# Optimization experiments

Measured on AMD Instinct MI355X. Metric: run time of the kernel, lower is better.

## Reference

```python
import jax, jax.numpy as jnp
import numpy as np

VEC, HID, B, S = 1280, 128, 4, 256
EPS = 1e-5


def _ln(x):
    m = x.mean(-1, keepdims=True)
    v = ((x - m) ** 2).mean(-1, keepdims=True)
    return (x - m) / jnp.sqrt(v + EPS)


def _add_attn(q_in, kv_in, Wq, Wk, wv):
    # Additive (Bahdanau) attention: scores[b,i,j] = wv . tanh(q[b,i] + k[b,j])
    q = q_in @ Wq            # [B, Sq, H]
    k = kv_in @ Wk           # [B, Sk, H]
    feat = jnp.tanh(q[:, :, None, :] + k[:, None, :, :])   # [B, Sq, Sk, H]
    scores = jnp.einsum('bijh,h->bij', feat, wv)
    attn = jax.nn.softmax(scores, axis=-1)
    return jnp.einsum('bij,bjd->bid', attn, kv_in)          # values = kv_in


def _res_fc(x, W1, b1, W2, b2):
    return jnp.maximum(x @ W1 + b1, 0.0) @ W2 + b2 + x


def setup_inputs() -> dict:
    key = jax.random.key(0)
    ks = iter(jax.random.split(key, 64))
    d = {
        'X': jax.random.normal(next(ks), (B, S, VEC), dtype=jnp.float32),
        'lys_pos': 100,
    }
    sc = 0.02
    for i in (1, 2, 3, 4):
        d[f'Wq{i}'] = jax.random.normal(next(ks), (VEC, HID), dtype=jnp.float32) * sc
        d[f'Wk{i}'] = jax.random.normal(next(ks), (VEC, HID), dtype=jnp.float32) * sc
        d[f'wv{i}'] = jax.random.normal(next(ks), (HID,), dtype=jnp.float32) * sc
    for i in (1, 2, 3):
        d[f'rW1_{i}'] = jax.random.normal(next(ks), (VEC, HID), dtype=jnp.float32) * sc
        d[f'rb1_{i}'] = jnp.zeros((HID,), dtype=jnp.float32)
        d[f'rW2_{i}'] = jax.random.normal(next(ks), (HID, VEC), dtype=jnp.float32) * sc
        d[f'rb2_{i}'] = jnp.zeros((VEC,), dtype=jnp.float32)
    d['hW1'] = jax.random.normal(next(ks), (VEC, 32), dtype=jnp.float32) * sc
    d['hb1'] = jnp.zeros((32,), dtype=jnp.float32)
    d['hW2'] = jax.random.normal(next(ks), (32, 12), dtype=jnp.float32) * sc
    d['hb2'] = jnp.zeros((12,), dtype=jnp.float32)
    d['hW3'] = jax.random.normal(next(ks), (12, 2), dtype=jnp.float32) * sc
    d['hb3'] = jnp.zeros((2,), dtype=jnp.float32)
    return d


def reference(X, lys_pos,
              Wq1, Wk1, wv1, Wq2, Wk2, wv2, Wq3, Wk3, wv3, Wq4, Wk4, wv4,
              rW1_1, rb1_1, rW2_1, rb2_1,
              rW1_2, rb1_2, rW2_2, rb2_2,
              rW1_3, rb1_3, rW2_3, rb2_3,
              hW1, hb1, hW2, hb2, hW3, hb3):
    X = X.astype(jnp.float32)
    X = _ln(_add_attn(X, X, Wq1, Wk1, wv1) + X)
    X = _res_fc(X, rW1_1, rb1_1, rW2_1, rb2_1)
    X = _ln(_add_attn(X, X, Wq2, Wk2, wv2) + X)
    X = _res_fc(X, rW1_2, rb1_2, rW2_2, rb2_2)
    X = _ln(_add_attn(X, X, Wq3, Wk3, wv3) + X)
    X = _res_fc(X, rW1_3, rb1_3, rW2_3, rb2_3)
    X_lys = X[:, lys_pos, :][:, None, :]                    # [B, 1, VEC]
    X_lys = _ln(_add_attn(X_lys, X, Wq4, Wk4, wv4) + X_lys)
    h = jnp.maximum(X_lys @ hW1 + hb1, 0.0)                 # dropout = identity (eval)
    h = jnp.maximum(h @ hW2 + hb2, 0.0)
    logits = (h @ hW3 + hb3)[:, 0, :]                       # squeeze(1) -> [B, 2]
    return logits
```

## Files before the change

kernel.cpp:

```cpp
#include <hip/hip_runtime.h>


#define DEV __device__ __forceinline__

static constexpr int VEC = 1280;
static constexpr int HID = 128;
static constexpr int BB  = 4;
static constexpr int SS  = 256;
static constexpr int MROWS = BB * SS;
static constexpr int NPART = 8;
static constexpr float INV_VEC = 1.0f / 1280.0f;

DEV float ftanh(float x) {
  float e = __expf(2.0f * x);
  return 1.0f - __fdividef(2.0f, e + 1.0f);
}

DEV float waveSum(float v) {
#pragma unroll
  for (int off = 32; off > 0; off >>= 1) v += __shfl_xor(v, off, 64);
  return v;
}
DEV float waveMax(float v) {
#pragma unroll
  for (int off = 32; off > 0; off >>= 1) v = fmaxf(v, __shfl_xor(v, off, 64));
  return v;
}
DEV float blockSum(float v, float* red) {
  v = waveSum(v);
  int tid = threadIdx.x;
  if ((tid & 63) == 0) red[tid >> 6] = v;
  __syncthreads();
  float r = (red[0] + red[1]) + (red[2] + red[3]);
  __syncthreads();
  return r;
}
DEV float blockMax(float v, float* red) {
  v = waveMax(v);
  int tid = threadIdx.x;
  if ((tid & 63) == 0) red[tid >> 6] = v;
  __syncthreads();
  float r = fmaxf(fmaxf(red[0], red[1]), fmaxf(red[2], red[3]));
  __syncthreads();
  return r;
}

template <int MODE, bool AFUSE, bool ALN, bool OBIAS, bool RESLN, bool RESP,
          bool STATS>
__global__ __launch_bounds__(256) void gemm_k(
    const float* __restrict__ A, long sAb, long aPart,
    const float* __restrict__ B0, const float* __restrict__ B1, int nSplitB,
    long sBb, int ldB,
    float* __restrict__ C, long sCb,
    const float* __restrict__ aBias, const float* __restrict__ oBias,
    const float* __restrict__ res,
    float* __restrict__ Ssum, float* __restrict__ Ssq,
    int N, int K, int kChunk) {
  const int n0 = blockIdx.x * 64;
  const int m0 = blockIdx.y * 64;
  const int z  = blockIdx.z;

  const float* Ab = A + (MODE == 2 ? (long)z * sAb : 0L);
  float*       Cb = C + (MODE >= 1 ? (long)z * sCb : 0L);
  const float* resb = (RESP || RESLN)
                          ? (res + (MODE == 2 ? (long)z * sCb : 0L))
                          : nullptr;
  const float* Bsel;
  int nb;
  if (n0 < nSplitB) { Bsel = B0; nb = n0; } else { Bsel = B1; nb = n0 - nSplitB; }
  if (MODE == 2) Bsel += (long)z * sBb;

  const int kBeg = (MODE == 1) ? z * kChunk : 0;
  const int kEnd = (MODE == 1) ? kBeg + kChunk : K;

  __shared__ float As[16][68];
  __shared__ float Bs[16][68];

  const int tid = threadIdx.x;
  const int tx = tid & 15, ty = tid >> 4;
  const int ar = tid >> 2, ac = (tid & 3) << 2;
  const int br = tid >> 4, bc = (tid & 15) << 2;

  float aMean = 0.0f, aRstd = 1.0f;
  if (ALN) {
    const int rm = m0 + ar;
    const float s = Ssum[rm], q = Ssq[rm];
    aMean = s * INV_VEC;
    aRstd = rsqrtf(q * INV_VEC - aMean * aMean + 1e-5f);
  }

  auto loadA = [&](int kt) -> float4 {
    const size_t off = (size_t)(m0 + ar) * K + kt + ac;
    float4 s = *(const float4*)(Ab + off);
    if (AFUSE) {
#pragma unroll
      for (int p2 = 1; p2 < NPART; ++p2) {
        const float4 t2 = *(const float4*)(Ab + (long)p2 * aPart + off);
        s.x += t2.x; s.y += t2.y; s.z += t2.z; s.w += t2.w;
      }
      const float4 bz = *(const float4*)(aBias + kt + ac);
      s.x = fmaxf(s.x + bz.x, 0.0f);
      s.y = fmaxf(s.y + bz.y, 0.0f);
      s.z = fmaxf(s.z + bz.z, 0.0f);
      s.w = fmaxf(s.w + bz.w, 0.0f);
    }
    if (ALN) {
      s.x = (s.x - aMean) * aRstd;
      s.y = (s.y - aMean) * aRstd;
      s.z = (s.z - aMean) * aRstd;
      s.w = (s.w - aMean) * aRstd;
    }
    return s;
  };
  auto loadB = [&](int kt) -> float4 {
    return *(const float4*)(Bsel + (size_t)(kt + br) * ldB + nb + bc);
  };

  float acc[4][4] = {};
  float4 a4 = loadA(kBeg);
  float4 b4 = loadB(kBeg);

  for (int kt = kBeg; kt < kEnd; kt += 16) {
    __syncthreads();
    As[ac + 0][ar] = a4.x;
    As[ac + 1][ar] = a4.y;
    As[ac + 2][ar] = a4.z;
    As[ac + 3][ar] = a4.w;
    *(float4*)&Bs[br][bc] = b4;
    __syncthreads();
    if (kt + 16 < kEnd) {
      a4 = loadA(kt + 16);
      b4 = loadB(kt + 16);
    }
#pragma unroll
    for (int kk = 0; kk < 16; ++kk) {
      const float4 av = *(const float4*)&As[kk][ty << 2];
      const float4 bv = *(const float4*)&Bs[kk][tx << 2];
      const float a[4] = {av.x, av.y, av.z, av.w};
      const float b[4] = {bv.x, bv.y, bv.z, bv.w};
#pragma unroll
      for (int i = 0; i < 4; ++i)
#pragma unroll
        for (int j = 0; j < 4; ++j) acc[i][j] = fmaf(a[i], b[j], acc[i][j]);
    }
  }

  float rs[4], rq[4];
#pragma unroll
  for (int i = 0; i < 4; ++i) {
    const int m = m0 + (ty << 2) + i;
    float mean = 0.0f, rstd = 1.0f;
    if (RESLN) {
      const float s = Ssum[m], q = Ssq[m];
      mean = s * INV_VEC;
      rstd = rsqrtf(q * INV_VEC - mean * mean + 1e-5f);
    }
    if (STATS) { rs[i] = 0.0f; rq[i] = 0.0f; }
#pragma unroll
    for (int j = 0; j < 4; ++j) {
      const int n = n0 + (tx << 2) + j;
      float v = acc[i][j];
      if (OBIAS) v += oBias[n];
      if (RESP) v += resb[(size_t)m * N + n];
      if (RESLN) v += (resb[(size_t)m * N + n] - mean) * rstd;
      Cb[(size_t)m * N + n] = v;
      if (STATS) { rs[i] += v; rq[i] = fmaf(v, v, rq[i]); }
    }
  }
  if (STATS) {
#pragma unroll
    for (int i = 0; i < 4; ++i) {
      float s = rs[i], q = rq[i];
#pragma unroll
      for (int msk = 1; msk < 16; msk <<= 1) {
        s += __shfl_xor(s, msk, 64);
        q += __shfl_xor(q, msk, 64);
      }
      if ((tid & 15) == 0) {
        const int rowg = (MODE == 2 ? z * SS : 0) + m0 + (ty << 2) + i;
        atomicAdd(&Ssum[rowg], s);
        atomicAdd(&Ssq[rowg], q);
      }
    }
  }
}

__global__ __launch_bounds__(256) void qksum_k(const float* __restrict__ QKp,
                                               long ps,
                                               float* __restrict__ Qd,
                                               float* __restrict__ KT,
                                               float* __restrict__ stats) {
  const int r = blockIdx.x, tid = threadIdx.x;
  if (r < 8) stats[r * 256 + tid] = 0.0f;
  const int b = r >> 8, j = r & 255;
  const size_t off = (size_t)r * 256 + tid;
  float v = 0.0f;
#pragma unroll
  for (int p = 0; p < NPART; ++p) v += QKp[(long)p * ps + off];
  if (tid < 128) {
    Qd[(size_t)r * 128 + tid] = v;
  } else {
    KT[(size_t)b * 32768 + (size_t)(tid - 128) * 256 + j] = v;
  }
}

__global__ __launch_bounds__(256) void scores2_k(const float* __restrict__ Qd,
                                                 const float* __restrict__ KT,
                                                 const float* __restrict__ wv,
                                                 float* __restrict__ attn) {
  const int b = blockIdx.y, i0 = blockIdx.x * 2, tid = threadIdx.x;
  __shared__ float qs[2][128], wvs[128], red[4];
  {
    const int rr = tid >> 7, h = tid & 127;
    qs[rr][h] = Qd[(size_t)(b * 256 + i0 + rr) * 128 + h];
  }
  if (tid < 128) wvs[tid] = wv[tid];
  __syncthreads();

  const float* KTb = KT + (size_t)b * 32768 + tid;
  float s0 = 0.0f, s1 = 0.0f;
#pragma unroll 4
  for (int h = 0; h < 128; h += 4) {
    const float k0 = KTb[(h + 0) * 256];
    const float k1 = KTb[(h + 1) * 256];
    const float k2 = KTb[(h + 2) * 256];
    const float k3 = KTb[(h + 3) * 256];
    const float w0 = wvs[h], w1 = wvs[h + 1], w2 = wvs[h + 2], w3 = wvs[h + 3];
    s0 += w0 * ftanh(qs[0][h] + k0) + w1 * ftanh(qs[0][h + 1] + k1) +
          w2 * ftanh(qs[0][h + 2] + k2) + w3 * ftanh(qs[0][h + 3] + k3);
    s1 += w0 * ftanh(qs[1][h] + k0) + w1 * ftanh(qs[1][h + 1] + k1) +
          w2 * ftanh(qs[1][h + 2] + k2) + w3 * ftanh(qs[1][h + 3] + k3);
  }
  {
    const float mx = blockMax(s0, red);
    const float e = __expf(s0 - mx);
    const float tot = blockSum(e, red);
    attn[(size_t)(b * 256 + i0) * 256 + tid] = e / tot;
  }
  {
    const float mx = blockMax(s1, red);
    const float e = __expf(s1 - mx);
    const float tot = blockSum(e, red);
    attn[(size_t)(b * 256 + i0 + 1) * 256 + tid] = e / tot;
  }
}

__global__ __launch_bounds__(256) void kt4q4_k(const float* __restrict__ K4p,
                                               const float* __restrict__ X3,
                                               const float* __restrict__ Wq4,
                                               const int* __restrict__ lys,
                                               float* __restrict__ KT,
                                               float* __restrict__ q4d) {
  __shared__ float partial[256];
  const int vb = blockIdx.x, tid = threadIdx.x;
  if (vb < 512) {
    const int r = vb * 2 + (tid >> 7), h = tid & 127;
    const int b = r >> 8, j = r & 255;
    const size_t off = (size_t)r * 128 + h;
    float v = 0.0f;
#pragma unroll
    for (int p = 0; p < NPART; ++p) v += K4p[(long)p * 131072 + off];
    KT[(size_t)b * 32768 + (size_t)h * 256 + j] = v;
  } else {
    const int b = vb - 512;
    const int lp = lys[0];
    const float* xr = X3 + (size_t)(b * 256 + lp) * VEC;
    const int h = tid & 127, half = tid >> 7;
    float acc = 0.0f;
    const int k0 = half * 640;
    for (int k = k0; k < k0 + 640; ++k)
      acc = fmaf(xr[k], Wq4[(size_t)k * HID + h], acc);
    partial[tid] = acc;
    __syncthreads();
    if (tid < 128) q4d[b * 128 + tid] = partial[tid] + partial[tid + 128];
  }
}

__global__ __launch_bounds__(256) void pv4s_k(const float* __restrict__ q4d,
                                              const float* __restrict__ KT,
                                              const float* __restrict__ wv4,
                                              const int* __restrict__ lys,
                                              const float* __restrict__ X3,
                                              float* __restrict__ A4) {
  const int b = blockIdx.x & 3, cs = blockIdx.x >> 2, tid = threadIdx.x;
  __shared__ float qs[128], wvs[128], aw[256], red[4];
  const int lp = lys[0];
  if (tid < 128) {
    qs[tid] = q4d[b * 128 + tid];
    wvs[tid] = wv4[tid];
  }
  __syncthreads();
  const float* KTb = KT + (size_t)b * 32768 + tid;
  float s = 0.0f;
#pragma unroll 4
  for (int h = 0; h < 128; h += 4) {
    s += wvs[h + 0] * ftanh(qs[h + 0] + KTb[(h + 0) * 256]);
    s += wvs[h + 1] * ftanh(qs[h + 1] + KTb[(h + 1) * 256]);
    s += wvs[h + 2] * ftanh(qs[h + 2] + KTb[(h + 2) * 256]);
    s += wvs[h + 3] * ftanh(qs[h + 3] + KTb[(h + 3) * 256]);
  }
  const float mx = blockMax(s, red);
  const float e = __expf(s - mx);
  const float tot = blockSum(e, red);
  aw[tid] = e / tot;
  __syncthreads();

  const int c = cs * 256 + tid;
  const float* Xb = X3 + (size_t)b * SS * VEC;
  float acc = 0.0f;
#pragma unroll 8
  for (int j = 0; j < 256; ++j) acc = fmaf(aw[j], Xb[(size_t)j * VEC + c], acc);
  acc += Xb[(size_t)lp * VEC + c];
  A4[b * VEC + c] = acc;
}

__global__ __launch_bounds__(256) void lnhead_k(
    const float* __restrict__ A4,
    const float* __restrict__ hW1, const float* __restrict__ hb1,
    const float* __restrict__ hW2, const float* __restrict__ hb2,
    const float* __restrict__ hW3, const float* __restrict__ hb3,
    float* __restrict__ out) {
  const int b = blockIdx.x, tid = threadIdx.x;
  __shared__ float xrow[1280], partial[256], red[4];
  __shared__ float h1s[32], h2s[12];
  float v[5];
  float sum = 0.0f;
#pragma unroll
  for (int k = 0; k < 5; ++k) {
    v[k] = A4[b * VEC + tid + k * 256];
    sum += v[k];
  }
  sum = blockSum(sum, red);
  const float m = sum * INV_VEC;
  float sq = 0.0f;
#pragma unroll
  for (int k = 0; k < 5; ++k) {
    const float dl = v[k] - m;
    sq += dl * dl;
  }
  sq = blockSum(sq, red);
  const float rstd = rsqrtf(sq * INV_VEC + 1e-5f);
#pragma unroll
  for (int k = 0; k < 5; ++k) xrow[tid + k * 256] = (v[k] - m) * rstd;
  __syncthreads();
  {
    const int n = tid & 31, sl = tid >> 5;
    float p = 0.0f;
    for (int k = sl * 160; k < sl * 160 + 160; ++k)
      p = fmaf(xrow[k], hW1[(size_t)k * 32 + n], p);
    partial[tid] = p;
  }
  __syncthreads();
  if (tid < 32) {
    float t = 0.0f;
#pragma unroll
    for (int s2 = 0; s2 < 8; ++s2) t += partial[s2 * 32 + tid];
    h1s[tid] = fmaxf(t + hb1[tid], 0.0f);
  }
  __syncthreads();
  if (tid < 12) {
    float t = 0.0f;
#pragma unroll
    for (int k = 0; k < 32; ++k) t = fmaf(h1s[k], hW2[k * 12 + tid], t);
    h2s[tid] = fmaxf(t + hb2[tid], 0.0f);
  }
  __syncthreads();
  if (tid < 2) {
    float t = 0.0f;
#pragma unroll
    for (int k = 0; k < 12; ++k) t = fmaf(h2s[k], hW3[k * 2 + tid], t);
    out[b * 2 + tid] = t + hb3[tid];
  }
}

extern "C" void kernel_launch(void* const* d_in, const int* in_sizes, int n_in,
                              void* d_out, int out_size, void* d_ws, size_t ws_size,
                              hipStream_t stream) {
  const float* X = (const float*)d_in[0];
  const int* lys = (const int*)d_in[1];
  const float* Wq[4] = {(const float*)d_in[2], (const float*)d_in[5],
                        (const float*)d_in[8], (const float*)d_in[11]};
  const float* Wk[4] = {(const float*)d_in[3], (const float*)d_in[6],
                        (const float*)d_in[9], (const float*)d_in[12]};
  const float* wv[4] = {(const float*)d_in[4], (const float*)d_in[7],
                        (const float*)d_in[10], (const float*)d_in[13]};
  const float* rW1[3] = {(const float*)d_in[14], (const float*)d_in[18],
                         (const float*)d_in[22]};
  const float* rb1[3] = {(const float*)d_in[15], (const float*)d_in[19],
                         (const float*)d_in[23]};
  const float* rW2[3] = {(const float*)d_in[16], (const float*)d_in[20],
                         (const float*)d_in[24]};
  const float* rb2[3] = {(const float*)d_in[17], (const float*)d_in[21],
                         (const float*)d_in[25]};
  const float* hW1 = (const float*)d_in[26];
  const float* hb1 = (const float*)d_in[27];
  const float* hW2 = (const float*)d_in[28];
  const float* hb2 = (const float*)d_in[29];
  const float* hW3 = (const float*)d_in[30];
  const float* hb3 = (const float*)d_in[31];
  float* out = (float*)d_out;

  float* ws = (float*)d_ws;
  const long QK_PS = 262144;
  const long H_PS  = 131072;
  float* QKp   = ws;
  float* Qd    = QKp + (long)NPART * QK_PS;
  float* KT    = Qd + 131072;
  float* attn  = KT + 131072;
  float* Yraw  = attn + 262144;
  float* Hp    = Yraw + 1310720;
  float* buf0  = Hp + (long)NPART * H_PS;
  float* buf1  = buf0 + 1310720;
  float* stats = buf1 + 1310720;
  float* q4d   = stats + 2048;
  float* A4    = q4d + 512;
  float* Ssum = stats, *Ssq = stats + 1024;

  const int NSPLIT_NONE = 1 << 30;
  const float* P[3] = {X, buf0, buf1};
  float* Q[3] = {buf0, buf1, buf0};

  for (int l = 0; l < 3; ++l) {
    const float* Xin = P[l];
    gemm_k<1, false, false, false, false, false, false>
        <<<dim3(4, 16, NPART), 256, 0, stream>>>(
            Xin, 0, 0, Wq[l], Wk[l], HID, 0, HID, QKp, QK_PS, nullptr, nullptr,
            nullptr, nullptr, nullptr, 256, VEC, 160);
    qksum_k<<<dim3(MROWS), 256, 0, stream>>>(QKp, QK_PS, Qd, KT, stats);
    scores2_k<<<dim3(128, BB), 256, 0, stream>>>(Qd, KT, wv[l], attn);
    gemm_k<2, false, false, false, false, true, true>
        <<<dim3(20, 4, BB), 256, 0, stream>>>(
            attn, (long)SS * SS, 0, Xin, Xin, NSPLIT_NONE, (long)SS * VEC, VEC,
            Yraw, (long)SS * VEC, nullptr, nullptr, Xin, Ssum, Ssq,
            VEC, SS, 0);
    gemm_k<1, false, true, false, false, false, false>
        <<<dim3(2, 16, NPART), 256, 0, stream>>>(
            Yraw, 0, 0, rW1[l], rW1[l], NSPLIT_NONE, 0, HID, Hp, H_PS, nullptr,
            nullptr, nullptr, Ssum, Ssq, HID, VEC, 160);
    gemm_k<0, true, false, true, true, false, false>
        <<<dim3(20, 16, 1), 256, 0, stream>>>(
            Hp, 0, H_PS, rW2[l], rW2[l], NSPLIT_NONE, 0, VEC, Q[l], 0, rb1[l],
            rb2[l], Yraw, Ssum, Ssq, VEC, HID, 0);
  }

  const float* X3 = Q[2];
  gemm_k<1, false, false, false, false, false, false>
      <<<dim3(2, 16, NPART), 256, 0, stream>>>(
          X3, 0, 0, Wk[3], Wk[3], NSPLIT_NONE, 0, HID, QKp, H_PS, nullptr,
          nullptr, nullptr, nullptr, nullptr, HID, VEC, 160);
  kt4q4_k<<<dim3(516), 256, 0, stream>>>(QKp, X3, Wq[3], lys, KT, q4d);
  pv4s_k<<<dim3(20), 256, 0, stream>>>(q4d, KT, wv[3], lys, X3, A4);
  lnhead_k<<<dim3(BB), 256, 0, stream>>>(A4, hW1, hb1, hW2, hb2, hW3, hb3, out);
}
```

Baseline: 454.2 us.

## Retune GEMM tiling, deepen split-K, atomically reduce the hidden GEMM

Templates the GEMM kernel on tile shape and per-thread micro-tile, so the attention-value and FC2 GEMMs can use smaller 64x32 and 32x64 tiles that launch more blocks. Split-K depth rises from 8 to 16 partitions. The FC1 GEMM now accumulates straight into one hidden buffer with atomicAdd; that buffer is zeroed inside qksum. This removes the 8-way partial-sum reads in the FC2 A-load. The scores kernel moves from two query rows per block to one, for more parallelism. The costs are more atomic traffic, more partial-buffer reads in qksum and kt4q4, and float summation order that now varies from run to run.

```diff
diff --git a/kernel.cpp b/kernel.cpp
--- a/kernel.cpp
+++ b/kernel.cpp
@@ -8,7 +8,7 @@
 static constexpr int BB  = 4;
 static constexpr int SS  = 256;
 static constexpr int MROWS = BB * SS;
-static constexpr int NPART = 8;
+static constexpr int NPART = 16;
 static constexpr float INV_VEC = 1.0f / 1280.0f;
 
 DEV float ftanh(float x) {
@@ -45,10 +45,10 @@
   return r;
 }
 
-template <int MODE, bool AFUSE, bool ALN, bool OBIAS, bool RESLN, bool RESP,
-          bool STATS>
+template <int TM, int TN, int MI, int NJ, int MODE, bool ABR, bool ALN,
+          bool OBIAS, bool RESLN, bool RESP, bool STATS, bool CATOMIC>
 __global__ __launch_bounds__(256) void gemm_k(
-    const float* __restrict__ A, long sAb, long aPart,
+    const float* __restrict__ A, long sAb,
     const float* __restrict__ B0, const float* __restrict__ B1, int nSplitB,
     long sBb, int ldB,
     float* __restrict__ C, long sCb,
@@ -56,8 +56,8 @@
     const float* __restrict__ res,
     float* __restrict__ Ssum, float* __restrict__ Ssq,
     int N, int K, int kChunk) {
-  const int n0 = blockIdx.x * 64;
-  const int m0 = blockIdx.y * 64;
+  const int n0 = blockIdx.x * TN;
+  const int m0 = blockIdx.y * TM;
   const int z  = blockIdx.z;
 
   const float* Ab = A + (MODE == 2 ? (long)z * sAb : 0L);
@@ -73,13 +73,15 @@
   const int kBeg = (MODE == 1) ? z * kChunk : 0;
   const int kEnd = (MODE == 1) ? kBeg + kChunk : K;
 
-  __shared__ float As[16][68];
-  __shared__ float Bs[16][68];
+  __shared__ float As[16][TM + 4];
+  __shared__ float Bs[16][TN + 4];
 
   const int tid = threadIdx.x;
   const int tx = tid & 15, ty = tid >> 4;
-  const int ar = tid >> 2, ac = (tid & 3) << 2;
-  const int br = tid >> 4, bc = (tid & 15) << 2;
+  const int ar = (TM == 64) ? (tid >> 2) : (tid >> 3);
+  const int ac = (TM == 64) ? ((tid & 3) << 2) : ((tid & 7) << 1);
+  const int br = tid >> 4;
+  const int bc = (TN == 64) ? ((tid & 15) << 2) : ((tid & 15) << 1);
 
   float aMean = 0.0f, aRstd = 1.0f;
   if (ALN) {
@@ -91,42 +93,67 @@
 
   auto loadA = [&](int kt) -> float4 {
     const size_t off = (size_t)(m0 + ar) * K + kt + ac;
-    float4 s = *(const float4*)(Ab + off);
-    if (AFUSE) {
-#pragma unroll
-      for (int p2 = 1; p2 < NPART; ++p2) {
-        const float4 t2 = *(const float4*)(Ab + (long)p2 * aPart + off);
-        s.x += t2.x; s.y += t2.y; s.z += t2.z; s.w += t2.w;
+    float4 r = {0, 0, 0, 0};
+    if constexpr (TM == 64) {
+      r = *(const float4*)(Ab + off);
+    } else {
+      const float2 t = *(const float2*)(Ab + off);
+      r.x = t.x; r.y = t.y;
+    }
+    if (ABR) {
+      if constexpr (TM == 64) {
+        const float4 bz = *(const float4*)(aBias + kt + ac);
+        r.x = fmaxf(r.x + bz.x, 0.0f);
+        r.y = fmaxf(r.y + bz.y, 0.0f);
+        r.z = fmaxf(r.z + bz.z, 0.0f);
+        r.w = fmaxf(r.w + bz.w, 0.0f);
+      } else {
+        const float2 bz = *(const float2*)(aBias + kt + ac);
+        r.x = fmaxf(r.x + bz.x, 0.0f);
+        r.y = fmaxf(r.y + bz.y, 0.0f);
       }
-      const float4 bz = *(const float4*)(aBias + kt + ac);
-      s.x = fmaxf(s.x + bz.x, 0.0f);
-      s.y = fmaxf(s.y + bz.y, 0.0f);
-      s.z = fmaxf(s.z + bz.z, 0.0f);
-      s.w = fmaxf(s.w + bz.w, 0.0f);
     }
     if (ALN) {
-      s.x = (s.x - aMean) * aRstd;
-      s.y = (s.y - aMean) * aRstd;
-      s.z = (s.z - aMean) * aRstd;
-      s.w = (s.w - aMean) * aRstd;
-    }
-    return s;
+      r.x = (r.x - aMean) * aRstd;
+      r.y = (r.y - aMean) * aRstd;
+      r.z = (r.z - aMean) * aRstd;
+      r.w = (r.w - aMean) * aRstd;
+    }
+    return r;
   };
   auto loadB = [&](int kt) -> float4 {
-    return *(const float4*)(Bsel + (size_t)(kt + br) * ldB + nb + bc);
+    const size_t off = (size_t)(kt + br) * ldB + nb + bc;
+    float4 r = {0, 0, 0, 0};
+    if constexpr (TN == 64) {
+      r = *(const float4*)(Bsel + off);
+    } else {
+      const float2 t = *(const float2*)(Bsel + off);
+      r.x = t.x; r.y = t.y;
+    }
+    return r;
   };
-
-  float acc[4][4] = {};
+  auto stage = [&](float4 a4, float4 b4) {
+    As[ac + 0][ar] = a4.x;
+    As[ac + 1][ar] = a4.y;
+    if constexpr (TM == 64) {
+      As[ac + 2][ar] = a4.z;
+      As[ac + 3][ar] = a4.w;
+    }
+    if constexpr (TN == 64) {
+      *(float4*)&Bs[br][bc] = b4;
+    } else {
+      Bs[br][bc] = b4.x;
+      Bs[br][bc + 1] = b4.y;
+    }
+  };
+
+  float acc[MI][NJ] = {};
   float4 a4 = loadA(kBeg);
   float4 b4 = loadB(kBeg);
 
   for (int kt = kBeg; kt < kEnd; kt += 16) {
     __syncthreads();
-    As[ac + 0][ar] = a4.x;
-    As[ac + 1][ar] = a4.y;
-    As[ac + 2][ar] = a4.z;
-    As[ac + 3][ar] = a4.w;
-    *(float4*)&Bs[br][bc] = b4;
+    stage(a4, b4);
     __syncthreads();
     if (kt + 16 < kEnd) {
       a4 = loadA(kt + 16);
@@ -134,52 +161,59 @@
     }
 #pragma unroll
     for (int kk = 0; kk < 16; ++kk) {
-      const float4 av = *(const float4*)&As[kk][ty << 2];
-      const float4 bv = *(const float4*)&Bs[kk][tx << 2];
-      const float a[4] = {av.x, av.y, av.z, av.w};
-      const float b[4] = {bv.x, bv.y, bv.z, bv.w};
-#pragma unroll
-      for (int i = 0; i < 4; ++i)
-#pragma unroll
-        for (int j = 0; j < 4; ++j) acc[i][j] = fmaf(a[i], b[j], acc[i][j]);
-    }
-  }
-
-  float rs[4], rq[4];
-#pragma unroll
-  for (int i = 0; i < 4; ++i) {
-    const int m = m0 + (ty << 2) + i;
+      float a[MI], b[NJ];
+      if constexpr (MI == 4) {
+        const float4 av = *(const float4*)&As[kk][ty << 2];
+        a[0] = av.x; a[1] = av.y; a[2] = av.z; a[3] = av.w;
+      } else {
+        const float2 av = *(const float2*)&As[kk][ty << 1];
+        a[0] = av.x; a[1] = av.y;
+      }
+      if constexpr (NJ == 4) {
+        const float4 bv = *(const float4*)&Bs[kk][tx << 2];
+        b[0] = bv.x; b[1] = bv.y; b[2] = bv.z; b[3] = bv.w;
+      } else {
+        const float2 bv = *(const float2*)&Bs[kk][tx << 1];
+        b[0] = bv.x; b[1] = bv.y;
+      }
+#pragma unroll
+      for (int i = 0; i < MI; ++i)
+#pragma unroll
+        for (int j = 0; j < NJ; ++j) acc[i][j] = fmaf(a[i], b[j], acc[i][j]);
+    }
+  }
+
+#pragma unroll
+  for (int i = 0; i < MI; ++i) {
+    const int m = m0 + ty * MI + i;
     float mean = 0.0f, rstd = 1.0f;
     if (RESLN) {
       const float s = Ssum[m], q = Ssq[m];
       mean = s * INV_VEC;
       rstd = rsqrtf(q * INV_VEC - mean * mean + 1e-5f);
     }
-    if (STATS) { rs[i] = 0.0f; rq[i] = 0.0f; }
-#pragma unroll
-    for (int j = 0; j < 4; ++j) {
-      const int n = n0 + (tx << 2) + j;
+    float rs = 0.0f, rq = 0.0f;
+#pragma unroll
+    for (int j = 0; j < NJ; ++j) {
+      const int n = n0 + tx * NJ + j;
       float v = acc[i][j];
       if (OBIAS) v += oBias[n];
       if (RESP) v += resb[(size_t)m * N + n];
       if (RESLN) v += (resb[(size_t)m * N + n] - mean) * rstd;
-      Cb[(size_t)m * N + n] = v;
-      if (STATS) { rs[i] += v; rq[i] = fmaf(v, v, rq[i]); }
-    }
-  }
-  if (STATS) {
-#pragma unroll
-    for (int i = 0; i < 4; ++i) {
-      float s = rs[i], q = rq[i];
+      if (CATOMIC) atomicAdd(&Cb[(size_t)m * N + n], v);
+      else Cb[(size_t)m * N + n] = v;
+      if (STATS) { rs += v; rq = fmaf(v, v, rq); }
+    }
+    if (STATS) {
 #pragma unroll
       for (int msk = 1; msk < 16; msk <<= 1) {
-        s += __shfl_xor(s, msk, 64);
-        q += __shfl_xor(q, msk, 64);
+        rs += __shfl_xor(rs, msk, 64);
+        rq += __shfl_xor(rq, msk, 64);
       }
       if ((tid & 15) == 0) {
-        const int rowg = (MODE == 2 ? z * SS : 0) + m0 + (ty << 2) + i;
-        atomicAdd(&Ssum[rowg], s);
-        atomicAdd(&Ssq[rowg], q);
+        const int rowg = (MODE == 2 ? z * SS : 0) + m;
+        atomicAdd(&Ssum[rowg], rs);
+        atomicAdd(&Ssq[rowg], rq);
       }
     }
   }
@@ -189,9 +223,11 @@
                                                long ps,
                                                float* __restrict__ Qd,
                                                float* __restrict__ KT,
+                                               float* __restrict__ Hd,
                                                float* __restrict__ stats) {
   const int r = blockIdx.x, tid = threadIdx.x;
   if (r < 8) stats[r * 256 + tid] = 0.0f;
+  if (tid < 128) Hd[(size_t)r * 128 + tid] = 0.0f;
   const int b = r >> 8, j = r & 255;
   const size_t off = (size_t)r * 256 + tid;
   float v = 0.0f;
@@ -204,45 +240,31 @@
   }
 }
 
-__global__ __launch_bounds__(256) void scores2_k(const float* __restrict__ Qd,
+__global__ __launch_bounds__(256) void scores1_k(const float* __restrict__ Qd,
                                                  const float* __restrict__ KT,
                                                  const float* __restrict__ wv,
                                                  float* __restrict__ attn) {
-  const int b = blockIdx.y, i0 = blockIdx.x * 2, tid = threadIdx.x;
-  __shared__ float qs[2][128], wvs[128], red[4];
-  {
-    const int rr = tid >> 7, h = tid & 127;
-    qs[rr][h] = Qd[(size_t)(b * 256 + i0 + rr) * 128 + h];
-  }
-  if (tid < 128) wvs[tid] = wv[tid];
+  const int b = blockIdx.y, i = blockIdx.x, tid = threadIdx.x;
+  __shared__ float qs[128], wvs[128], red[4];
+  if (tid < 128) {
+    qs[tid] = Qd[(size_t)(b * 256 + i) * 128 + tid];
+    wvs[tid] = wv[tid];
+  }
   __syncthreads();
 
   const float* KTb = KT + (size_t)b * 32768 + tid;
-  float s0 = 0.0f, s1 = 0.0f;
+  float s = 0.0f;
 #pragma unroll 4
   for (int h = 0; h < 128; h += 4) {
-    const float k0 = KTb[(h + 0) * 256];
-    const float k1 = KTb[(h + 1) * 256];
-    const float k2 = KTb[(h + 2) * 256];
-    const float k3 = KTb[(h + 3) * 256];
-    const float w0 = wvs[h], w1 = wvs[h + 1], w2 = wvs[h + 2], w3 = wvs[h + 3];
-    s0 += w0 * ftanh(qs[0][h] + k0) + w1 * ftanh(qs[0][h + 1] + k1) +
-          w2 * ftanh(qs[0][h + 2] + k2) + w3 * ftanh(qs[0][h + 3] + k3);
-    s1 += w0 * ftanh(qs[1][h] + k0) + w1 * ftanh(qs[1][h + 1] + k1) +
-          w2 * ftanh(qs[1][h + 2] + k2) + w3 * ftanh(qs[1][h + 3] + k3);
-  }
-  {
-    const float mx = blockMax(s0, red);
-    const float e = __expf(s0 - mx);
-    const float tot = blockSum(e, red);
-    attn[(size_t)(b * 256 + i0) * 256 + tid] = e / tot;
-  }
-  {
-    const float mx = blockMax(s1, red);
-    const float e = __expf(s1 - mx);
-    const float tot = blockSum(e, red);
-    attn[(size_t)(b * 256 + i0 + 1) * 256 + tid] = e / tot;
-  }
+    s += wvs[h + 0] * ftanh(qs[h + 0] + KTb[(h + 0) * 256]);
+    s += wvs[h + 1] * ftanh(qs[h + 1] + KTb[(h + 1) * 256]);
+    s += wvs[h + 2] * ftanh(qs[h + 2] + KTb[(h + 2) * 256]);
+    s += wvs[h + 3] * ftanh(qs[h + 3] + KTb[(h + 3) * 256]);
+  }
+  const float mx = blockMax(s, red);
+  const float e = __expf(s - mx);
+  const float tot = blockSum(e, red);
+  attn[(size_t)(b * 256 + i) * 256 + tid] = e / tot;
 }
 
 __global__ __launch_bounds__(256) void kt4q4_k(const float* __restrict__ K4p,
@@ -408,8 +430,8 @@
   float* KT    = Qd + 131072;
   float* attn  = KT + 131072;
   float* Yraw  = attn + 262144;
-  float* Hp    = Yraw + 1310720;
-  float* buf0  = Hp + (long)NPART * H_PS;
+  float* Hd    = Yraw + 1310720;
+  float* buf0  = Hd + 131072;
   float* buf1  = buf0 + 1310720;
   float* stats = buf1 + 1310720;
   float* q4d   = stats + 2048;
@@ -422,32 +444,32 @@
 
   for (int l = 0; l < 3; ++l) {
     const float* Xin = P[l];
-    gemm_k<1, false, false, false, false, false, false>
+    gemm_k<64, 64, 4, 4, 1, false, false, false, false, false, false, false>
         <<<dim3(4, 16, NPART), 256, 0, stream>>>(
-            Xin, 0, 0, Wq[l], Wk[l], HID, 0, HID, QKp, QK_PS, nullptr, nullptr,
-            nullptr, nullptr, nullptr, 256, VEC, 160);
-    qksum_k<<<dim3(MROWS), 256, 0, stream>>>(QKp, QK_PS, Qd, KT, stats);
-    scores2_k<<<dim3(128, BB), 256, 0, stream>>>(Qd, KT, wv[l], attn);
-    gemm_k<2, false, false, false, false, true, true>
-        <<<dim3(20, 4, BB), 256, 0, stream>>>(
-            attn, (long)SS * SS, 0, Xin, Xin, NSPLIT_NONE, (long)SS * VEC, VEC,
+            Xin, 0, Wq[l], Wk[l], HID, 0, HID, QKp, QK_PS, nullptr, nullptr,
+            nullptr, nullptr, nullptr, 256, VEC, 80);
+    qksum_k<<<dim3(MROWS), 256, 0, stream>>>(QKp, QK_PS, Qd, KT, Hd, stats);
+    scores1_k<<<dim3(SS, BB), 256, 0, stream>>>(Qd, KT, wv[l], attn);
+    gemm_k<64, 32, 4, 2, 2, false, false, false, false, true, true, false>
+        <<<dim3(40, 4, BB), 256, 0, stream>>>(
+            attn, (long)SS * SS, Xin, Xin, NSPLIT_NONE, (long)SS * VEC, VEC,
             Yraw, (long)SS * VEC, nullptr, nullptr, Xin, Ssum, Ssq,
             VEC, SS, 0);
-    gemm_k<1, false, true, false, false, false, false>
+    gemm_k<64, 64, 4, 4, 1, false, true, false, false, false, false, true>
         <<<dim3(2, 16, NPART), 256, 0, stream>>>(
-            Yraw, 0, 0, rW1[l], rW1[l], NSPLIT_NONE, 0, HID, Hp, H_PS, nullptr,
-            nullptr, nullptr, Ssum, Ssq, HID, VEC, 160);
-    gemm_k<0, true, false, true, true, false, false>
-        <<<dim3(20, 16, 1), 256, 0, stream>>>(
-            Hp, 0, H_PS, rW2[l], rW2[l], NSPLIT_NONE, 0, VEC, Q[l], 0, rb1[l],
+            Yraw, 0, rW1[l], rW1[l], NSPLIT_NONE, 0, HID, Hd, 0, nullptr,
+            nullptr, nullptr, Ssum, Ssq, HID, VEC, 80);
+    gemm_k<32, 64, 2, 4, 0, true, false, true, true, false, false, false>
+        <<<dim3(20, 32, 1), 256, 0, stream>>>(
+            Hd, 0, rW2[l], rW2[l], NSPLIT_NONE, 0, VEC, Q[l], 0, rb1[l],
             rb2[l], Yraw, Ssum, Ssq, VEC, HID, 0);
   }
 
   const float* X3 = Q[2];
-  gemm_k<1, false, false, false, false, false, false>
+  gemm_k<64, 64, 4, 4, 1, false, false, false, false, false, false, false>
       <<<dim3(2, 16, NPART), 256, 0, stream>>>(
-          X3, 0, 0, Wk[3], Wk[3], NSPLIT_NONE, 0, HID, QKp, H_PS, nullptr,
-          nullptr, nullptr, nullptr, nullptr, HID, VEC, 160);
+          X3, 0, Wk[3], Wk[3], NSPLIT_NONE, 0, HID, QKp, H_PS, nullptr,
+          nullptr, nullptr, nullptr, nullptr, HID, VEC, 80);
   kt4q4_k<<<dim3(516), 256, 0, stream>>>(QKp, X3, Wq[3], lys, KT, q4d);
   pv4s_k<<<dim3(20), 256, 0, stream>>>(q4d, KT, wv[3], lys, X3, A4);
   lnhead_k<<<dim3(BB), 256, 0, stream>>>(A4, hW1, hb1, hW2, hb2, hW3, hb3, out);
```

After: 490.8 us. 8.1% more time.
